# Optimization experiments

Hardware: AMD Instinct MI355X
Metric: run time of the kernel (lower is better)

## Reference

```python
import jax, jax.numpy as jnp
import numpy as np

DIM = 512
KEY_DIM = 32
NUM_HEADS = 8
ATTN_RATIO = 4
RES = 1024
B = 16
NH_KD = KEY_DIM * NUM_HEADS          # 256
D = ATTN_RATIO * KEY_DIM             # 128
DH = D * NUM_HEADS                   # 1024
H_QKV = DH + 2 * NH_KD               # 1536
EPS = 1e-5
SCALE = KEY_DIM ** -0.5


def bn(y, g, b, m, v):
    # eval-mode BatchNorm1d over channel dim of [B, C, L]
    inv = g / jnp.sqrt(v + EPS)
    return (y - m[None, :, None]) * inv[None, :, None] + b[None, :, None]


def setup_inputs() -> dict:
    key = jax.random.key(0)
    ks = jax.random.split(key, 16)
    x = jax.random.normal(ks[0], (B, DIM, RES), dtype=jnp.float32)
    w_qkv = jax.random.normal(ks[1], (H_QKV, DIM), dtype=jnp.float32) * 0.02
    qkv_g = jnp.ones((H_QKV,), jnp.float32)
    qkv_b = jnp.zeros((H_QKV,), jnp.float32)
    qkv_m = jax.random.normal(ks[2], (H_QKV,), jnp.float32) * 0.1
    qkv_v = jax.random.uniform(ks[3], (H_QKV,), jnp.float32) + 0.5
    w_dw = jax.random.normal(ks[4], (NH_KD, 1, 3), jnp.float32) * 0.1
    dw_g = jnp.ones((NH_KD,), jnp.float32)
    dw_b = jnp.zeros((NH_KD,), jnp.float32)
    dw_m = jax.random.normal(ks[5], (NH_KD,), jnp.float32) * 0.1
    dw_v = jax.random.uniform(ks[6], (NH_KD,), jnp.float32) + 0.5
    w_proj = jax.random.normal(ks[7], (DIM, DH), jnp.float32) * 0.02
    proj_g = jnp.ones((DIM,), jnp.float32)  # bn_weight_init=0 in source, use 1 for nontrivial output
    proj_b = jnp.zeros((DIM,), jnp.float32)
    proj_m = jax.random.normal(ks[8], (DIM,), jnp.float32) * 0.1
    proj_v = jax.random.uniform(ks[9], (DIM,), jnp.float32) + 0.5
    attention_biases = jax.random.normal(ks[10], (NUM_HEADS, RES), jnp.float32) * 0.02
    pts = jnp.arange(RES)
    bias_idxs = jnp.abs(pts[:, None] - pts[None, :]).astype(jnp.int32)  # [N, N]
    return dict(x=x, w_qkv=w_qkv, qkv_g=qkv_g, qkv_b=qkv_b, qkv_m=qkv_m, qkv_v=qkv_v,
                w_dw=w_dw, dw_g=dw_g, dw_b=dw_b, dw_m=dw_m, dw_v=dw_v,
                w_proj=w_proj, proj_g=proj_g, proj_b=proj_b, proj_m=proj_m, proj_v=proj_v,
                attention_biases=attention_biases, bias_idxs=bias_idxs)


def reference(x, w_qkv, qkv_g, qkv_b, qkv_m, qkv_v,
              w_dw, dw_g, dw_b, dw_m, dw_v,
              w_proj, proj_g, proj_b, proj_m, proj_v,
              attention_biases, bias_idxs):
    Bsz, _, L = x.shape
    # qkv: conv1x1 + BN
    qkv = bn(jnp.einsum('bcl,oc->bol', x, w_qkv), qkv_g, qkv_b, qkv_m, qkv_v)
    q = qkv[:, :NH_KD]
    k = qkv[:, NH_KD:2 * NH_KD]
    v = qkv[:, 2 * NH_KD:]
    # depthwise conv k=3 pad=1 on q, then BN
    q = jax.lax.conv_general_dilated(q, w_dw, window_strides=(1,), padding=((1, 1),),
                                     dimension_numbers=('NCH', 'OIH', 'NCH'),
                                     feature_group_count=NH_KD)
    q = bn(q, dw_g, dw_b, dw_m, dw_v)
    q = q.reshape(Bsz, NUM_HEADS, KEY_DIM, L)
    k = k.reshape(Bsz, NUM_HEADS, KEY_DIM, L)
    v = v.reshape(Bsz, NUM_HEADS, D, L)
    ab = attention_biases[:, bias_idxs]  # [H, N, N]
    attn = jnp.einsum('bhdn,bhdm->bhnm', q, k) * SCALE + ab[None]
    attn = jax.nn.softmax(attn, axis=-1)
    out = jnp.einsum('bhdm,bhnm->bhdn', v, attn).reshape(Bsz, DH, L)
    # proj: ReLU -> conv1x1 -> BN
    out = jax.nn.relu(out)
    out = bn(jnp.einsum('bcl,oc->bol', out, w_proj), proj_g, proj_b, proj_m, proj_v)
    return out
```

## Files before the change

kernel.cpp:

```cpp
#include <hip/hip_runtime.h>
#include <stdint.h>

#define DEV __device__ __forceinline__

typedef unsigned short u16;
typedef __bf16 bf16x8 __attribute__((ext_vector_type(8)));
typedef float floatx4 __attribute__((ext_vector_type(4)));
typedef unsigned short u16x4 __attribute__((ext_vector_type(4)));
typedef unsigned short u16x8 __attribute__((ext_vector_type(8)));
typedef short s16x4 __attribute__((ext_vector_type(4)));


DEV u16 f2bf(float x) {
  union { float f; uint32_t u; } v; v.f = x;
  uint32_t r = v.u + 0x7FFFu + ((v.u >> 16) & 1u);
  return (u16)(r >> 16);
}
DEV float bf2f(u16 x) {
  union { uint32_t u; float f; } v; v.u = ((uint32_t)x) << 16;
  return v.f;
}
DEV float loadf(const void* p, int i, int bf) {
  return bf ? bf2f(((const u16*)p)[i]) : ((const float*)p)[i];
}
DEV u16 fastbf(float x) {
  union { float f; uint32_t u; } v; v.f = x;
  return (u16)((v.u + 0x8000u) >> 16);
}

DEV floatx4 mfma16(bf16x8 a, bf16x8 b, floatx4 c) {
  return __builtin_amdgcn_mfma_f32_16x16x32_bf16(a, b, c, 0, 0, 0);
}

#if __has_builtin(__builtin_amdgcn_mfma_f32_16x16x16bf16_1k)
DEV floatx4 mfma16k16(s16x4 a, s16x4 b, floatx4 c) {
  return __builtin_amdgcn_mfma_f32_16x16x16bf16_1k(a, b, c, 0, 0, 0);
}
#elif __has_builtin(__builtin_amdgcn_mfma_f32_16x16x16_bf16)
DEV floatx4 mfma16k16(s16x4 a, s16x4 b, floatx4 c) {
  return __builtin_amdgcn_mfma_f32_16x16x16_bf16(a, b, c, 0, 0, 0);
}
#else
DEV floatx4 mfma16k16(s16x4 a, s16x4 b, floatx4 c) {
  asm volatile("v_mfma_f32_16x16x16_bf16 %0, %1, %2, %0"
               : "+v"(c) : "v"(a), "v"(b));
  return c;
}
#endif

DEV void gl_lds16(const void* g, void* l) {
  __builtin_amdgcn_global_load_lds(
      (const __attribute__((address_space(1))) void*)g,
      (__attribute__((address_space(3))) void*)l, 16, 0, 0);
}

__global__ void sniff(const uint32_t* __restrict__ x, int* __restrict__ flag) {
  int lane = threadIdx.x & 63;
  int hits = 0;
#pragma unroll
  for (int i = 0; i < 4; ++i) {
    uint32_t u = x[lane * 4 + i];
    int e = (u >> 7) & 0xFF;
    hits += (e >= 100 && e <= 140) ? 1 : 0;
  }
  unsigned long long m = __ballot(hits >= 3);
  if (lane == 0) *flag = (__popcll(m) >= 40) ? 1 : 0;
}

__global__ __launch_bounds__(256) void cvt_all(
    const void* __restrict__ a, const void* __restrict__ b,
    const void* __restrict__ c, const void* __restrict__ d,
    u16* __restrict__ oa, u16* __restrict__ ob, u16* __restrict__ oc,
    u16* __restrict__ od, const int* __restrict__ flag) {
  int i = blockIdx.x * 256 + threadIdx.x;
  int bf = *flag;
  if (i < 786432) {
    oa[i] = bf ? ((const u16*)a)[i] : f2bf(((const float*)a)[i]);
  } else if (i < 1310720) {
    int j = i - 786432;
    ob[j] = bf ? ((const u16*)b)[j] : f2bf(((const float*)b)[j]);
  } else if (i < 1311488) {
    int j = i - 1310720;
    oc[j] = bf ? ((const u16*)c)[j] : f2bf(((const float*)c)[j]);
  } else if (i < 1319680) {
    int j = i - 1311488;
    od[j] = bf ? ((const u16*)d)[j] : f2bf(((const float*)d)[j]);
  }
}

__global__ __launch_bounds__(256) void prep_params(
    const void* qg, const void* qb, const void* qm, const void* qv,
    const void* dg, const void* db, const void* dm, const void* dv,
    const void* pg, const void* pb, const void* pm, const void* pv,
    float* scl, float* shf, const int* __restrict__ flag) {
  int i = blockIdx.x * 256 + threadIdx.x;
  if (i >= 2304) return;
  int bf = *flag;
  float g, b, m, v;
  if (i < 1536)      { g = loadf(qg, i, bf); b = loadf(qb, i, bf); m = loadf(qm, i, bf); v = loadf(qv, i, bf); }
  else if (i < 1792) { int j = i - 1536; g = loadf(dg, j, bf); b = loadf(db, j, bf); m = loadf(dm, j, bf); v = loadf(dv, j, bf); }
  else               { int j = i - 1792; g = loadf(pg, j, bf); b = loadf(pb, j, bf); m = loadf(pm, j, bf); v = loadf(pv, j, bf); }
  float s = g / sqrtf(v + 1e-5f);
  scl[i] = s;
  shf[i] = b - m * s;
}

__global__ __launch_bounds__(256) void transpose_x(const void* __restrict__ x,
                                                   u16* __restrict__ xT,
                                                   const int* __restrict__ flag) {
  __shared__ __align__(16) u16 tile[64 * 72];
  const int tid = threadIdx.x;
  const int b = blockIdx.z, c0 = blockIdx.y * 64, l0 = blockIdx.x * 64;
  const int bf = *flag;
  const size_t base = ((size_t)b * 512 + c0) * 1024 + l0;
  if (bf) {
    const u16* xb = (const u16*)x + base;
#pragma unroll
    for (int it = 0; it < 4; ++it) {
      int flat = it * 256 + tid;
      int row = flat >> 4, c4 = flat & 15;
      u16x4 v = *(const u16x4*)(xb + (size_t)row * 1024 + c4 * 4);
      tile[(c4 * 4 + 0) * 72 + row] = v.x;
      tile[(c4 * 4 + 1) * 72 + row] = v.y;
      tile[(c4 * 4 + 2) * 72 + row] = v.z;
      tile[(c4 * 4 + 3) * 72 + row] = v.w;
    }
  } else {
    const float* xb = (const float*)x + base;
#pragma unroll
    for (int it = 0; it < 4; ++it) {
      int flat = it * 256 + tid;
      int row = flat >> 4, c4 = flat & 15;
      floatx4 v = *(const floatx4*)(xb + (size_t)row * 1024 + c4 * 4);
      tile[(c4 * 4 + 0) * 72 + row] = f2bf(v[0]);
      tile[(c4 * 4 + 1) * 72 + row] = f2bf(v[1]);
      tile[(c4 * 4 + 2) * 72 + row] = f2bf(v[2]);
      tile[(c4 * 4 + 3) * 72 + row] = f2bf(v[3]);
    }
  }
  __syncthreads();
  u16* xTb = xT + ((size_t)b * 1024 + l0) * 512 + c0;
#pragma unroll
  for (int it = 0; it < 4; ++it) {
    int flat = it * 256 + tid;
    int row = flat >> 4, c4 = flat & 15;
    u16x4 v = *(const u16x4*)&tile[row * 72 + c4 * 4];
    *(u16x4*)(xTb + (size_t)row * 512 + c4 * 4) = v;
  }
}

template <int K>
__global__ __launch_bounds__(256) void gemm_bn(
    const u16* __restrict__ A, const u16* __restrict__ BT, u16* __restrict__ Y,
    const float* __restrict__ scl, const float* __restrict__ shf, int sclOff,
    const int* __restrict__ flag, int outFlagged) {
  __shared__ __align__(16) u16 lds[4 * 64 * 72];
  const int tid = threadIdx.x, lane = tid & 63, w = tid >> 6;
  const int l15 = lane & 15, quad = lane >> 4;
  const int o_blk = blockIdx.y * 128, l_blk = blockIdx.x * 128, b = blockIdx.z;
  const int o_off = (w >> 1) * 64, l_off = (w & 1) * 64;
  const u16* BTb = BT + (size_t)b * 1024 * K;

  floatx4 acc[4][4];
#pragma unroll
  for (int i = 0; i < 4; ++i)
#pragma unroll
    for (int j = 0; j < 4; ++j) acc[i][j] = (floatx4){0.f, 0.f, 0.f, 0.f};

  for (int k0 = 0; k0 < K; k0 += 32) {
    __syncthreads();
#pragma unroll
    for (int s = 0; s < 2; ++s) {
      const int chunk = (s * 4 + w) * 1024;
      const int byteoff = chunk + lane * 16;
      const int row = byteoff >> 6;
      const int col = (byteoff & 63) >> 1;
      gl_lds16(A + (size_t)(o_blk + row) * K + k0 + col, &lds[chunk >> 1]);
      gl_lds16(BTb + (size_t)(l_blk + row) * K + k0 + col, &lds[4096 + (chunk >> 1)]);
    }
    __syncthreads();
    bf16x8 af[4], bfr[4];
#pragma unroll
    for (int ir = 0; ir < 4; ++ir)
      af[ir] = *(const bf16x8*)&lds[(o_off + 16 * ir + l15) * 32 + quad * 8];
#pragma unroll
    for (int jc = 0; jc < 4; ++jc)
      bfr[jc] = *(const bf16x8*)&lds[4096 + (l_off + 16 * jc + l15) * 32 + quad * 8];
#pragma unroll
    for (int ir = 0; ir < 4; ++ir)
#pragma unroll
      for (int jc = 0; jc < 4; ++jc)
        acc[ir][jc] = mfma16(af[ir], bfr[jc], acc[ir][jc]);
  }
  __syncthreads();
  u16* eb = &lds[w * 4608];
#pragma unroll
  for (int ir = 0; ir < 4; ++ir) {
#pragma unroll
    for (int r = 0; r < 4; ++r) {
      int rloc = 16 * ir + quad * 4 + r;
      int o = o_blk + o_off + rloc;
      float s = scl[sclOff + o], hh = shf[sclOff + o];
#pragma unroll
      for (int jc = 0; jc < 4; ++jc)
        eb[rloc * 72 + 16 * jc + l15] = f2bf(acc[ir][jc][r] * s + hh);
    }
  }
  asm volatile("s_waitcnt lgkmcnt(0)" ::: "memory");
  const int M = gridDim.y * 128;
  const size_t ybase = ((size_t)b * M + o_blk + o_off) * 1024 + l_blk + l_off;
  const int outbf = outFlagged ? *flag : 1;
  if (outbf) {
#pragma unroll
    for (int it = 0; it < 8; ++it) {
      int flat = it * 64 + lane;
      int row = flat >> 3, g = flat & 7;
      u16x8 v = *(const u16x8*)&eb[row * 72 + g * 8];
      *(u16x8*)(Y + ybase + (size_t)row * 1024 + g * 8) = v;
    }
  } else {
    float* Yf = (float*)Y;
#pragma unroll
    for (int it = 0; it < 8; ++it) {
      int flat = it * 64 + lane;
      int row = flat >> 3, g = flat & 7;
      u16x8 v = *(const u16x8*)&eb[row * 72 + g * 8];
      floatx4 lo, hi;
#pragma unroll
      for (int t = 0; t < 4; ++t) { lo[t] = bf2f(v[t]); hi[t] = bf2f(v[4 + t]); }
      *(floatx4*)(Yf + ybase + (size_t)row * 1024 + g * 8) = lo;
      *(floatx4*)(Yf + ybase + (size_t)row * 1024 + g * 8 + 4) = hi;
    }
  }
}

__global__ __launch_bounds__(256) void dwconv_pack(
    const u16* __restrict__ qkv, const u16* __restrict__ w_dw,
    const float* __restrict__ scl, const float* __restrict__ shf,
    u16* __restrict__ qT, u16* __restrict__ kT) {
  __shared__ __align__(16) u16 lds[256 * 36];
  const int tid = threadIdx.x;
  const int lch = blockIdx.x, h = blockIdx.y, b = blockIdx.z;
  const int r = tid >> 3, seg = tid & 7;
  const int l0 = lch * 256 + seg * 32;
  {
    const int o = h * 32 + r;
    const u16* base = qkv + ((size_t)b * 1536 + o) * 1024;
    float w0 = bf2f(w_dw[o * 3 + 0]), w1 = bf2f(w_dw[o * 3 + 1]), w2 = bf2f(w_dw[o * 3 + 2]);
    float sc = scl[1536 + o], sh = shf[1536 + o];
    float prev = (l0 > 0) ? bf2f(base[l0 - 1]) : 0.f;
    float cur = bf2f(base[l0]);
#pragma unroll 4
    for (int j = 0; j < 32; ++j) {
      int lg = l0 + j;
      float nxt = (lg + 1 < 1024) ? bf2f(base[lg + 1]) : 0.f;
      lds[(seg * 32 + j) * 36 + r] = f2bf((w0 * prev + w1 * cur + w2 * nxt) * sc + sh);
      prev = cur; cur = nxt;
    }
  }
  __syncthreads();
  {
    const size_t qTb = (((size_t)b * 8 + h) * 1024 + lch * 256) * 32;
#pragma unroll
    for (int it = 0; it < 8; ++it) {
      int flat = it * 256 + tid;
      int ll = flat >> 3, g = flat & 7;
      u16x4 v = *(const u16x4*)&lds[ll * 36 + g * 4];
      *(u16x4*)(qT + qTb + (size_t)ll * 32 + g * 4) = v;
    }
  }
  __syncthreads();
  {
    const int o = 256 + h * 32 + r;
    const u16* base = qkv + ((size_t)b * 1536 + o) * 1024;
#pragma unroll 8
    for (int j = 0; j < 32; ++j) lds[(seg * 32 + j) * 36 + r] = base[l0 + j];
  }
  __syncthreads();
  {
    const size_t kTb = (((size_t)b * 8 + h) * 1024 + lch * 256) * 32;
#pragma unroll
    for (int it = 0; it < 8; ++it) {
      int flat = it * 256 + tid;
      int ll = flat >> 3, g = flat & 7;
      u16x4 v = *(const u16x4*)&lds[ll * 36 + g * 4];
      *(u16x4*)(kT + kTb + (size_t)ll * 32 + g * 4) = v;
    }
  }
}

__global__ __launch_bounds__(256) void attn(
    const u16* __restrict__ qT, const u16* __restrict__ kT,
    const u16* __restrict__ qkv, const u16* __restrict__ ab,
    u16* __restrict__ OT) {
  __shared__ __align__(16) float biasE[2048];
  __shared__ __align__(16) u16 ldsV[2 * 4096];
  const int tid = threadIdx.x, lane = tid & 63, w = tid >> 6;
  const int l15 = lane & 15, quad = lane >> 4;
  const int id = blockIdx.x;
  const int pair = id & 127, nb = id >> 7;
  const int b = pair >> 3, h = pair & 7;
  for (int i = tid; i < 2048; i += 256) {
    int d = i - 1024;
    int idx = d < 0 ? -d : d;
    if (idx > 1023) idx = 1023;
    biasE[i] = bf2f(ab[h * 1024 + idx]) * 1.44269504088896340f;
  }
  const int n0 = nb * 128 + w * 32;
  const size_t bh = ((size_t)b * 8 + h) * 1024;
  const u16* kTb = kT + bh * 32;
  const u16* vb = qkv + ((size_t)b * 1536 + 512 + h * 128) * 1024;
  const bf16x8 qf0 = *(const bf16x8*)(qT + bh * 32 + (size_t)(n0 + l15) * 32 + quad * 8);
  const bf16x8 qf1 = *(const bf16x8*)(qT + bh * 32 + (size_t)(n0 + 16 + l15) * 32 + quad * 8);
  const int srow = lane >> 2, sc = lane & 3;
  const int d0 = w * 32 + srow, d1 = d0 + 16;
  const u16* sg0 = vb + (size_t)d0 * 1024 + sc * 8;
  const u16* sg1 = vb + (size_t)d1 * 1024 + sc * 8;
  const int wb0 = (((d0 >> 4) * 4 + 2 * (sc & 1)) * 16 + (d0 & 15)) * 8 + (sc >> 1) * 4;
  const int wb1 = (((d1 >> 4) * 4 + 2 * (sc & 1)) * 16 + (d1 & 15)) * 8 + (sc >> 1) * 4;

  floatx4 oacc[2][8];
#pragma unroll
  for (int i = 0; i < 2; ++i)
#pragma unroll
    for (int j = 0; j < 8; ++j) oacc[i][j] = (floatx4){0.f, 0.f, 0.f, 0.f};
  float rs0 = 0.f, rs1 = 0.f;
  constexpr float c1 = 0.17677669529663689f * 1.44269504088896340f;
  const floatx4 zf = (floatx4){0.f, 0.f, 0.f, 0.f};

  {
    u16x8 a0 = *(const u16x8*)sg0;
    u16x8 a1 = *(const u16x8*)sg1;
    *(u16x4*)&ldsV[wb0]       = (u16x4){a0[0], a0[1], a0[2], a0[3]};
    *(u16x4*)&ldsV[wb0 + 128] = (u16x4){a0[4], a0[5], a0[6], a0[7]};
    *(u16x4*)&ldsV[wb1]       = (u16x4){a1[0], a1[1], a1[2], a1[3]};
    *(u16x4*)&ldsV[wb1 + 128] = (u16x4){a1[4], a1[5], a1[6], a1[7]};
  }
  __syncthreads();

  for (int m0 = 0; m0 < 1024; m0 += 32) {
    const int par = (m0 >> 5) & 1;
    const bool more = (m0 + 32) < 1024;
    u16x8 a0, a1;
    if (more) {
      a0 = *(const u16x8*)(sg0 + m0 + 32);
      a1 = *(const u16x8*)(sg1 + m0 + 32);
    }
    bf16x8 kf0 = *(const bf16x8*)(kTb + (size_t)(m0 + l15) * 32 + quad * 8);
    bf16x8 kf1 = *(const bf16x8*)(kTb + (size_t)(m0 + 16 + l15) * 32 + quad * 8);
    floatx4 s00 = mfma16(kf0, qf0, zf);
    floatx4 s10 = mfma16(kf1, qf0, zf);
    floatx4 s01 = mfma16(kf0, qf1, zf);
    floatx4 s11 = mfma16(kf1, qf1, zf);
    const int Cb = 1024 + n0 + l15 - quad * 4 - m0;
    float bm[4], b0v[4], bpv[4];
#pragma unroll
    for (int r = 0; r < 4; ++r) {
      bm[r]  = biasE[Cb - 16 - r];
      b0v[r] = biasE[Cb - r];
      bpv[r] = biasE[Cb + 16 - r];
    }
    s16x4 pf00, pf01, pf10, pf11;
#pragma unroll
    for (int r = 0; r < 4; ++r) {
      float p00 = __builtin_amdgcn_exp2f(s00[r] * c1 + b0v[r]);
      float p01 = __builtin_amdgcn_exp2f(s10[r] * c1 + bm[r]);
      float p10 = __builtin_amdgcn_exp2f(s01[r] * c1 + bpv[r]);
      float p11 = __builtin_amdgcn_exp2f(s11[r] * c1 + b0v[r]);
      rs0 += p00 + p01;
      rs1 += p10 + p11;
      pf00[r] = (short)fastbf(p00);
      pf01[r] = (short)fastbf(p01);
      pf10[r] = (short)fastbf(p10);
      pf11[r] = (short)fastbf(p11);
    }
    const int rbase = par * 4096 + quad * 128 + l15 * 8;
#pragma unroll
    for (int jd = 0; jd < 8; ++jd) {
      u16x8 vv = *(const u16x8*)&ldsV[rbase + jd * 512];
      s16x4 v0 = {(short)vv[0], (short)vv[1], (short)vv[2], (short)vv[3]};
      s16x4 v1 = {(short)vv[4], (short)vv[5], (short)vv[6], (short)vv[7]};
      oacc[0][jd] = mfma16k16(v0, pf00, oacc[0][jd]);
      oacc[0][jd] = mfma16k16(v1, pf01, oacc[0][jd]);
      oacc[1][jd] = mfma16k16(v0, pf10, oacc[1][jd]);
      oacc[1][jd] = mfma16k16(v1, pf11, oacc[1][jd]);
    }
    if (more) {
      u16* dst = ldsV + (par ^ 1) * 4096;
      *(u16x4*)&dst[wb0]       = (u16x4){a0[0], a0[1], a0[2], a0[3]};
      *(u16x4*)&dst[wb0 + 128] = (u16x4){a0[4], a0[5], a0[6], a0[7]};
      *(u16x4*)&dst[wb1]       = (u16x4){a1[0], a1[1], a1[2], a1[3]};
      *(u16x4*)&dst[wb1 + 128] = (u16x4){a1[4], a1[5], a1[6], a1[7]};
    }
    __syncthreads();
  }
  rs0 += __shfl_xor(rs0, 16, 64);
  rs0 += __shfl_xor(rs0, 32, 64);
  rs1 += __shfl_xor(rs1, 16, 64);
  rs1 += __shfl_xor(rs1, 32, 64);
  const float inv0 = __builtin_amdgcn_rcpf(rs0);
  const float inv1 = __builtin_amdgcn_rcpf(rs1);
  u16* OTb = OT + ((size_t)b * 1024 + n0 + l15) * 1024 + h * 128 + quad * 4;
#pragma unroll
  for (int jd = 0; jd < 8; ++jd) {
    u16x4 o0, o1;
#pragma unroll
    for (int r = 0; r < 4; ++r) {
      float v0 = oacc[0][jd][r] * inv0;
      float v1 = oacc[1][jd][r] * inv1;
      o0[r] = fastbf(v0 > 0.f ? v0 : 0.f);
      o1[r] = fastbf(v1 > 0.f ? v1 : 0.f);
    }
    *(u16x4*)(OTb + 16 * jd) = o0;
    *(u16x4*)(OTb + 16 * 1024 + 16 * jd) = o1;
  }
}

extern "C" void kernel_launch(void* const* d_in, const int* in_sizes, int n_in,
                              void* d_out, int out_size, void* d_ws, size_t ws_size,
                              hipStream_t stream) {
  const void* x      = d_in[0];
  const void* w_qkv  = d_in[1];
  const void* qkv_g  = d_in[2];
  const void* qkv_b  = d_in[3];
  const void* qkv_m  = d_in[4];
  const void* qkv_v  = d_in[5];
  const void* w_dw   = d_in[6];
  const void* dw_g   = d_in[7];
  const void* dw_b   = d_in[8];
  const void* dw_m   = d_in[9];
  const void* dw_v   = d_in[10];
  const void* w_proj = d_in[11];
  const void* proj_g = d_in[12];
  const void* proj_b = d_in[13];
  const void* proj_m = d_in[14];
  const void* proj_v = d_in[15];
  const void* abias  = d_in[16];

  char* ws = (char*)d_ws;
  u16*   xT      = (u16*)(ws);
  u16*   qkv     = (u16*)(ws + 16777216);
  u16*   qT      = (u16*)(ws + 67108864);
  u16*   kT      = (u16*)(ws + 75497472);
  u16*   OT      = (u16*)(ws + 83886080);
  float* scl     = (float*)(ws + 117440512);
  float* shf     = (float*)(ws + 117449728);
  u16*   wqkv_c  = (u16*)(ws + 117458944);
  u16*   wproj_c = (u16*)(ws + 119031808);
  u16*   wdw_c   = (u16*)(ws + 120080384);
  u16*   ab_c    = (u16*)(ws + 120082432);
  int*   flag    = (int*)(ws + 120098816);
  if (ws_size < (size_t)120098880) return;

  sniff<<<1, 64, 0, stream>>>((const uint32_t*)x, flag);
  cvt_all<<<5155, 256, 0, stream>>>(w_qkv, w_proj, w_dw, abias,
                                    wqkv_c, wproj_c, wdw_c, ab_c, flag);
  prep_params<<<9, 256, 0, stream>>>(qkv_g, qkv_b, qkv_m, qkv_v, dw_g, dw_b, dw_m,
                                     dw_v, proj_g, proj_b, proj_m, proj_v, scl, shf, flag);
  transpose_x<<<dim3(16, 8, 16), 256, 0, stream>>>(x, xT, flag);
  gemm_bn<512><<<dim3(8, 12, 16), 256, 0, stream>>>(wqkv_c, xT, qkv, scl, shf, 0, flag, 0);
  dwconv_pack<<<dim3(4, 8, 16), 256, 0, stream>>>(qkv, wdw_c, scl, shf, qT, kT);
  attn<<<1024, 256, 0, stream>>>(qT, kT, qkv, ab_c, OT);
  gemm_bn<1024><<<dim3(8, 4, 16), 256, 0, stream>>>(wproj_c, OT, (u16*)d_out, scl, shf, 1792, flag, 1);
}
```

Baseline: 282.3 us.

## Unroll attention loop by two with K prefetch, packed bf16 converts, and setprio

Restructures the attention inner loop into pairs of 32-column chunks with compile-time LDS buffer selection. The K fragments for the next chunk are prefetched from global memory before the current chunk is computed, which hides their load latency. Probabilities are converted with the hardware packed bf16 convert instruction instead of the software rounding routine. The PV MFMA block is raised in wave priority. This adds register pressure, and the bf16 rounding may differ slightly from before.

```diff
diff --git a/kernel.cpp b/kernel.cpp
--- a/kernel.cpp
+++ b/kernel.cpp
@@ -47,6 +47,13 @@
   return c;
 }
 #endif
+
+DEV s16x4 pk4(float a, float b, float c, float d) {
+  union { uint32_t u[2]; s16x4 v; } r;
+  asm("v_cvt_pk_bf16_f32 %0, %1, %2" : "=v"(r.u[0]) : "v"(a), "v"(b));
+  asm("v_cvt_pk_bf16_f32 %0, %1, %2" : "=v"(r.u[1]) : "v"(c), "v"(d));
+  return r.v;
+}
 
 DEV void gl_lds16(const void* g, void* l) {
   __builtin_amdgcn_global_load_lds(
@@ -328,53 +335,33 @@
   constexpr float c1 = 0.17677669529663689f * 1.44269504088896340f;
   const floatx4 zf = (floatx4){0.f, 0.f, 0.f, 0.f};
 
-  {
-    u16x8 a0 = *(const u16x8*)sg0;
-    u16x8 a1 = *(const u16x8*)sg1;
-    *(u16x4*)&ldsV[wb0]       = (u16x4){a0[0], a0[1], a0[2], a0[3]};
-    *(u16x4*)&ldsV[wb0 + 128] = (u16x4){a0[4], a0[5], a0[6], a0[7]};
-    *(u16x4*)&ldsV[wb1]       = (u16x4){a1[0], a1[1], a1[2], a1[3]};
-    *(u16x4*)&ldsV[wb1 + 128] = (u16x4){a1[4], a1[5], a1[6], a1[7]};
-  }
-  __syncthreads();
-
-  for (int m0 = 0; m0 < 1024; m0 += 32) {
-    const int par = (m0 >> 5) & 1;
-    const bool more = (m0 + 32) < 1024;
-    u16x8 a0, a1;
-    if (more) {
-      a0 = *(const u16x8*)(sg0 + m0 + 32);
-      a1 = *(const u16x8*)(sg1 + m0 + 32);
-    }
-    bf16x8 kf0 = *(const bf16x8*)(kTb + (size_t)(m0 + l15) * 32 + quad * 8);
-    bf16x8 kf1 = *(const bf16x8*)(kTb + (size_t)(m0 + 16 + l15) * 32 + quad * 8);
-    floatx4 s00 = mfma16(kf0, qf0, zf);
-    floatx4 s10 = mfma16(kf1, qf0, zf);
-    floatx4 s01 = mfma16(kf0, qf1, zf);
-    floatx4 s11 = mfma16(kf1, qf1, zf);
+  const u16* kfp = kTb + (size_t)l15 * 32 + quad * 8;
+
+  auto chunk = [&](bf16x8 kc0, bf16x8 kc1, int bufsel, int m0) {
+    floatx4 s00 = mfma16(kc0, qf0, zf);
+    floatx4 s10 = mfma16(kc1, qf0, zf);
+    floatx4 s01 = mfma16(kc0, qf1, zf);
+    floatx4 s11 = mfma16(kc1, qf1, zf);
     const int Cb = 1024 + n0 + l15 - quad * 4 - m0;
-    float bm[4], b0v[4], bpv[4];
+    float p00[4], p01[4], p10[4], p11[4];
 #pragma unroll
     for (int r = 0; r < 4; ++r) {
-      bm[r]  = biasE[Cb - 16 - r];
-      b0v[r] = biasE[Cb - r];
-      bpv[r] = biasE[Cb + 16 - r];
-    }
-    s16x4 pf00, pf01, pf10, pf11;
-#pragma unroll
-    for (int r = 0; r < 4; ++r) {
-      float p00 = __builtin_amdgcn_exp2f(s00[r] * c1 + b0v[r]);
-      float p01 = __builtin_amdgcn_exp2f(s10[r] * c1 + bm[r]);
-      float p10 = __builtin_amdgcn_exp2f(s01[r] * c1 + bpv[r]);
-      float p11 = __builtin_amdgcn_exp2f(s11[r] * c1 + b0v[r]);
-      rs0 += p00 + p01;
-      rs1 += p10 + p11;
-      pf00[r] = (short)fastbf(p00);
-      pf01[r] = (short)fastbf(p01);
-      pf10[r] = (short)fastbf(p10);
-      pf11[r] = (short)fastbf(p11);
-    }
-    const int rbase = par * 4096 + quad * 128 + l15 * 8;
+      float bm = biasE[Cb - 16 - r];
+      float b0 = biasE[Cb - r];
+      float bp = biasE[Cb + 16 - r];
+      p00[r] = __builtin_amdgcn_exp2f(s00[r] * c1 + b0);
+      p01[r] = __builtin_amdgcn_exp2f(s10[r] * c1 + bm);
+      p10[r] = __builtin_amdgcn_exp2f(s01[r] * c1 + bp);
+      p11[r] = __builtin_amdgcn_exp2f(s11[r] * c1 + b0);
+      rs0 += p00[r] + p01[r];
+      rs1 += p10[r] + p11[r];
+    }
+    s16x4 pf00 = pk4(p00[0], p00[1], p00[2], p00[3]);
+    s16x4 pf01 = pk4(p01[0], p01[1], p01[2], p01[3]);
+    s16x4 pf10 = pk4(p10[0], p10[1], p10[2], p10[3]);
+    s16x4 pf11 = pk4(p11[0], p11[1], p11[2], p11[3]);
+    const int rbase = bufsel * 4096 + quad * 128 + l15 * 8;
+    __builtin_amdgcn_s_setprio(1);
 #pragma unroll
     for (int jd = 0; jd < 8; ++jd) {
       u16x8 vv = *(const u16x8*)&ldsV[rbase + jd * 512];
@@ -385,12 +372,53 @@
       oacc[1][jd] = mfma16k16(v0, pf10, oacc[1][jd]);
       oacc[1][jd] = mfma16k16(v1, pf11, oacc[1][jd]);
     }
-    if (more) {
-      u16* dst = ldsV + (par ^ 1) * 4096;
+    __builtin_amdgcn_s_setprio(0);
+  };
+
+  bf16x8 ke0 = *(const bf16x8*)(kfp);
+  bf16x8 ke1 = *(const bf16x8*)(kfp + 16 * 32);
+  bf16x8 ko0, ko1;
+  {
+    u16x8 a0 = *(const u16x8*)sg0;
+    u16x8 a1 = *(const u16x8*)sg1;
+    *(u16x4*)&ldsV[wb0]       = (u16x4){a0[0], a0[1], a0[2], a0[3]};
+    *(u16x4*)&ldsV[wb0 + 128] = (u16x4){a0[4], a0[5], a0[6], a0[7]};
+    *(u16x4*)&ldsV[wb1]       = (u16x4){a1[0], a1[1], a1[2], a1[3]};
+    *(u16x4*)&ldsV[wb1 + 128] = (u16x4){a1[4], a1[5], a1[6], a1[7]};
+  }
+  __syncthreads();
+
+#pragma unroll 1
+  for (int mc = 0; mc < 1024; mc += 64) {
+    {
+      u16x8 a0 = *(const u16x8*)(sg0 + mc + 32);
+      u16x8 a1 = *(const u16x8*)(sg1 + mc + 32);
+      ko0 = *(const bf16x8*)(kfp + (size_t)(mc + 32) * 32);
+      ko1 = *(const bf16x8*)(kfp + (size_t)(mc + 48) * 32);
+      chunk(ke0, ke1, 0, mc);
+      u16* dst = ldsV + 4096;
       *(u16x4*)&dst[wb0]       = (u16x4){a0[0], a0[1], a0[2], a0[3]};
       *(u16x4*)&dst[wb0 + 128] = (u16x4){a0[4], a0[5], a0[6], a0[7]};
       *(u16x4*)&dst[wb1]       = (u16x4){a1[0], a1[1], a1[2], a1[3]};
       *(u16x4*)&dst[wb1 + 128] = (u16x4){a1[4], a1[5], a1[6], a1[7]};
+    }
+    __syncthreads();
+    {
+      const bool more = (mc + 64) < 1024;
+      u16x8 a0, a1;
+      if (more) {
+        a0 = *(const u16x8*)(sg0 + mc + 64);
+        a1 = *(const u16x8*)(sg1 + mc + 64);
+        ke0 = *(const bf16x8*)(kfp + (size_t)(mc + 64) * 32);
+        ke1 = *(const bf16x8*)(kfp + (size_t)(mc + 80) * 32);
+      }
+      chunk(ko0, ko1, 1, mc + 32);
+      if (more) {
+        *(u16x4*)&ldsV[wb0]       = (u16x4){a0[0], a0[1], a0[2], a0[3]};
+        *(u16x4*)&ldsV[wb0 + 128] = (u16x4){a0[4], a0[5], a0[6], a0[7]};
+        *(u16x4*)&ldsV[wb1]       = (u16x4){a1[0], a1[1], a1[2], a1[3]};
+        *(u16x4*)&ldsV[wb1 + 128] = (u16x4){a1[4], a1[5], a1[6], a1[7]};
+      }
     }
     __syncthreads();
   }
```

New measurement: 282.5 us. Within noise of the previous version (+0.1%).

## Split attention work across 8 waves of 16 query rows each

Applied to the files above, without the earlier changes.

The attention kernel goes from 4 waves handling 32 query rows each to 8 waves handling 16 rows each, with 512 threads per block. Per-wave accumulator state is halved, which frees registers and should raise occupancy and latency hiding. Each thread now stages one V row instead of two into LDS, and launch bounds request 4 blocks per CU. In exchange, each K fragment loaded feeds half as many MFMAs, so K global loads and bias LDS reads per unit of work roughly double, and barriers now synchronize twice as many waves.

```diff
diff --git a/kernel.cpp b/kernel.cpp
--- a/kernel.cpp
+++ b/kernel.cpp
@@ -289,7 +289,7 @@
   }
 }
 
-__global__ __launch_bounds__(256) void attn(
+__global__ __launch_bounds__(512, 4) void attn(
     const u16* __restrict__ qT, const u16* __restrict__ kT,
     const u16* __restrict__ qkv, const u16* __restrict__ ab,
     u16* __restrict__ OT) {
@@ -300,79 +300,58 @@
   const int id = blockIdx.x;
   const int pair = id & 127, nb = id >> 7;
   const int b = pair >> 3, h = pair & 7;
-  for (int i = tid; i < 2048; i += 256) {
-    int d = i - 1024;
-    int idx = d < 0 ? -d : d;
+  for (int i = tid; i < 2048; i += 512) {
+    int dd = i - 1024;
+    int idx = dd < 0 ? -dd : dd;
     if (idx > 1023) idx = 1023;
     biasE[i] = bf2f(ab[h * 1024 + idx]) * 1.44269504088896340f;
   }
-  const int n0 = nb * 128 + w * 32;
+  const int n0 = nb * 128 + w * 16;
   const size_t bh = ((size_t)b * 8 + h) * 1024;
   const u16* kTb = kT + bh * 32;
   const u16* vb = qkv + ((size_t)b * 1536 + 512 + h * 128) * 1024;
-  const bf16x8 qf0 = *(const bf16x8*)(qT + bh * 32 + (size_t)(n0 + l15) * 32 + quad * 8);
-  const bf16x8 qf1 = *(const bf16x8*)(qT + bh * 32 + (size_t)(n0 + 16 + l15) * 32 + quad * 8);
-  const int srow = lane >> 2, sc = lane & 3;
-  const int d0 = w * 32 + srow, d1 = d0 + 16;
-  const u16* sg0 = vb + (size_t)d0 * 1024 + sc * 8;
-  const u16* sg1 = vb + (size_t)d1 * 1024 + sc * 8;
-  const int wb0 = (((d0 >> 4) * 4 + 2 * (sc & 1)) * 16 + (d0 & 15)) * 8 + (sc >> 1) * 4;
-  const int wb1 = (((d1 >> 4) * 4 + 2 * (sc & 1)) * 16 + (d1 & 15)) * 8 + (sc >> 1) * 4;
-
-  floatx4 oacc[2][8];
-#pragma unroll
-  for (int i = 0; i < 2; ++i)
-#pragma unroll
-    for (int j = 0; j < 8; ++j) oacc[i][j] = (floatx4){0.f, 0.f, 0.f, 0.f};
-  float rs0 = 0.f, rs1 = 0.f;
+  const bf16x8 qf = *(const bf16x8*)(qT + bh * 32 + (size_t)(n0 + l15) * 32 + quad * 8);
+  const int d = tid >> 2, sc = tid & 3;
+  const u16* sg = vb + (size_t)d * 1024 + sc * 8;
+  const int wb = (((d >> 4) * 4 + 2 * (sc & 1)) * 16 + (d & 15)) * 8 + (sc >> 1) * 4;
+
+  floatx4 oacc[8];
+#pragma unroll
+  for (int j = 0; j < 8; ++j) oacc[j] = (floatx4){0.f, 0.f, 0.f, 0.f};
+  float rs = 0.f;
   constexpr float c1 = 0.17677669529663689f * 1.44269504088896340f;
   const floatx4 zf = (floatx4){0.f, 0.f, 0.f, 0.f};
 
+  const u16* kfp = kTb + (size_t)l15 * 32 + quad * 8;
+
   {
-    u16x8 a0 = *(const u16x8*)sg0;
-    u16x8 a1 = *(const u16x8*)sg1;
-    *(u16x4*)&ldsV[wb0]       = (u16x4){a0[0], a0[1], a0[2], a0[3]};
-    *(u16x4*)&ldsV[wb0 + 128] = (u16x4){a0[4], a0[5], a0[6], a0[7]};
-    *(u16x4*)&ldsV[wb1]       = (u16x4){a1[0], a1[1], a1[2], a1[3]};
-    *(u16x4*)&ldsV[wb1 + 128] = (u16x4){a1[4], a1[5], a1[6], a1[7]};
-  }
-  __syncthreads();
-
+    u16x8 a = *(const u16x8*)sg;
+    *(u16x4*)&ldsV[wb]       = (u16x4){a[0], a[1], a[2], a[3]};
+    *(u16x4*)&ldsV[wb + 128] = (u16x4){a[4], a[5], a[6], a[7]};
+  }
+  __syncthreads();
+
+#pragma unroll 1
   for (int m0 = 0; m0 < 1024; m0 += 32) {
     const int par = (m0 >> 5) & 1;
     const bool more = (m0 + 32) < 1024;
-    u16x8 a0, a1;
+    u16x8 a;
     if (more) {
-      a0 = *(const u16x8*)(sg0 + m0 + 32);
-      a1 = *(const u16x8*)(sg1 + m0 + 32);
-    }
-    bf16x8 kf0 = *(const bf16x8*)(kTb + (size_t)(m0 + l15) * 32 + quad * 8);
-    bf16x8 kf1 = *(const bf16x8*)(kTb + (size_t)(m0 + 16 + l15) * 32 + quad * 8);
-    floatx4 s00 = mfma16(kf0, qf0, zf);
-    floatx4 s10 = mfma16(kf1, qf0, zf);
-    floatx4 s01 = mfma16(kf0, qf1, zf);
-    floatx4 s11 = mfma16(kf1, qf1, zf);
+      a = *(const u16x8*)(sg + m0 + 32);
+    }
+    bf16x8 kf0 = *(const bf16x8*)(kfp + (size_t)m0 * 32);
+    bf16x8 kf1 = *(const bf16x8*)(kfp + (size_t)(m0 + 16) * 32);
+    floatx4 s0 = mfma16(kf0, qf, zf);
+    floatx4 s1 = mfma16(kf1, qf, zf);
     const int Cb = 1024 + n0 + l15 - quad * 4 - m0;
-    float bm[4], b0v[4], bpv[4];
+    s16x4 pf0, pf1;
 #pragma unroll
     for (int r = 0; r < 4; ++r) {
-      bm[r]  = biasE[Cb - 16 - r];
-      b0v[r] = biasE[Cb - r];
-      bpv[r] = biasE[Cb + 16 - r];
-    }
-    s16x4 pf00, pf01, pf10, pf11;
-#pragma unroll
-    for (int r = 0; r < 4; ++r) {
-      float p00 = __builtin_amdgcn_exp2f(s00[r] * c1 + b0v[r]);
-      float p01 = __builtin_amdgcn_exp2f(s10[r] * c1 + bm[r]);
-      float p10 = __builtin_amdgcn_exp2f(s01[r] * c1 + bpv[r]);
-      float p11 = __builtin_amdgcn_exp2f(s11[r] * c1 + b0v[r]);
-      rs0 += p00 + p01;
-      rs1 += p10 + p11;
-      pf00[r] = (short)fastbf(p00);
-      pf01[r] = (short)fastbf(p01);
-      pf10[r] = (short)fastbf(p10);
-      pf11[r] = (short)fastbf(p11);
+      float p0 = __builtin_amdgcn_exp2f(s0[r] * c1 + biasE[Cb - r]);
+      float p1 = __builtin_amdgcn_exp2f(s1[r] * c1 + biasE[Cb - 16 - r]);
+      rs += p0 + p1;
+      pf0[r] = (short)fastbf(p0);
+      pf1[r] = (short)fastbf(p1);
     }
     const int rbase = par * 4096 + quad * 128 + l15 * 8;
 #pragma unroll
@@ -380,39 +359,29 @@
       u16x8 vv = *(const u16x8*)&ldsV[rbase + jd * 512];
       s16x4 v0 = {(short)vv[0], (short)vv[1], (short)vv[2], (short)vv[3]};
       s16x4 v1 = {(short)vv[4], (short)vv[5], (short)vv[6], (short)vv[7]};
-      oacc[0][jd] = mfma16k16(v0, pf00, oacc[0][jd]);
-      oacc[0][jd] = mfma16k16(v1, pf01, oacc[0][jd]);
-      oacc[1][jd] = mfma16k16(v0, pf10, oacc[1][jd]);
-      oacc[1][jd] = mfma16k16(v1, pf11, oacc[1][jd]);
+      oacc[jd] = mfma16k16(v0, pf0, oacc[jd]);
+      oacc[jd] = mfma16k16(v1, pf1, oacc[jd]);
     }
     if (more) {
       u16* dst = ldsV + (par ^ 1) * 4096;
-      *(u16x4*)&dst[wb0]       = (u16x4){a0[0], a0[1], a0[2], a0[3]};
-      *(u16x4*)&dst[wb0 + 128] = (u16x4){a0[4], a0[5], a0[6], a0[7]};
-      *(u16x4*)&dst[wb1]       = (u16x4){a1[0], a1[1], a1[2], a1[3]};
-      *(u16x4*)&dst[wb1 + 128] = (u16x4){a1[4], a1[5], a1[6], a1[7]};
+      *(u16x4*)&dst[wb]       = (u16x4){a[0], a[1], a[2], a[3]};
+      *(u16x4*)&dst[wb + 128] = (u16x4){a[4], a[5], a[6], a[7]};
     }
     __syncthreads();
   }
-  rs0 += __shfl_xor(rs0, 16, 64);
-  rs0 += __shfl_xor(rs0, 32, 64);
-  rs1 += __shfl_xor(rs1, 16, 64);
-  rs1 += __shfl_xor(rs1, 32, 64);
-  const float inv0 = __builtin_amdgcn_rcpf(rs0);
-  const float inv1 = __builtin_amdgcn_rcpf(rs1);
+  rs += __shfl_xor(rs, 16, 64);
+  rs += __shfl_xor(rs, 32, 64);
+  const float inv = __builtin_amdgcn_rcpf(rs);
   u16* OTb = OT + ((size_t)b * 1024 + n0 + l15) * 1024 + h * 128 + quad * 4;
 #pragma unroll
   for (int jd = 0; jd < 8; ++jd) {
-    u16x4 o0, o1;
+    u16x4 o;
 #pragma unroll
     for (int r = 0; r < 4; ++r) {
-      float v0 = oacc[0][jd][r] * inv0;
-      float v1 = oacc[1][jd][r] * inv1;
-      o0[r] = fastbf(v0 > 0.f ? v0 : 0.f);
-      o1[r] = fastbf(v1 > 0.f ? v1 : 0.f);
-    }
-    *(u16x4*)(OTb + 16 * jd) = o0;
-    *(u16x4*)(OTb + 16 * 1024 + 16 * jd) = o1;
+      float v = oacc[jd][r] * inv;
+      o[r] = fastbf(v > 0.f ? v : 0.f);
+    }
+    *(u16x4*)(OTb + 16 * jd) = o;
   }
 }
 
@@ -460,6 +429,6 @@
   transpose_x<<<dim3(16, 8, 16), 256, 0, stream>>>(x, xT, flag);
   gemm_bn<512><<<dim3(8, 12, 16), 256, 0, stream>>>(wqkv_c, xT, qkv, scl, shf, 0, flag, 0);
   dwconv_pack<<<dim3(4, 8, 16), 256, 0, stream>>>(qkv, wdw_c, scl, shf, qT, kT);
-  attn<<<1024, 256, 0, stream>>>(qT, kT, qkv, ab_c, OT);
+  attn<<<1024, 512, 0, stream>>>(qT, kT, qkv, ab_c, OT);
   gemm_bn<1024><<<dim3(8, 4, 16), 256, 0, stream>>>(wproj_c, OT, (u16*)d_out, scl, shf, 1792, flag, 1);
 }
```

Result: faster. 274.0 us (-2.9%).
